# Optimization experiments

Measured on AMD Instinct MI355X. Metric: run time of the kernel, lower is better.

## Reference

```python
import jax, jax.numpy as jnp
import numpy as np

VOCAB, EMB, HID, OUT = 1000, 256, 512, 1
NUM_IN, NUM_OUT = 7, 4
B, S = 64, 512
D = EMB + NUM_OUT  # conv input dim = 260


def setup_inputs() -> dict:
    key = jax.random.key(0)
    ks = jax.random.split(key, 8)
    ev = jax.random.randint(ks[0], (B, S, 1), 0, VOCAB).astype(jnp.float32)
    num = jax.random.normal(ks[1], (B, S, NUM_IN), jnp.float32)
    X = jnp.concatenate([ev, num], axis=-1)  # [B,S,8]; col 0 = event ids
    def w(k, shape, fan_in):
        return jax.random.normal(k, shape, jnp.float32) / np.sqrt(fan_in).astype(np.float32)
    return {
        "X": X,
        "emb": w(ks[2], (VOCAB, EMB), EMB),
        "Wn": w(ks[3], (NUM_IN, NUM_OUT), NUM_IN), "bn": jnp.zeros((NUM_OUT,), jnp.float32),
        "Wf": w(ks[4], (D, 3 * HID), D), "bf": jnp.zeros((3 * HID,), jnp.float32),
        "Wb": w(ks[5], (D, 3 * HID), D), "bb": jnp.zeros((3 * HID,), jnp.float32),
        "Wo": w(ks[6], (2 * HID, OUT), 2 * HID), "bo": jnp.zeros((OUT,), jnp.float32),
    }


def _fo_pool(Z, F):
    # Z, F: [S, B, H]. Linear recurrence h_t = F_t * h_{t-1} + (1 - F_t) * Z_t.
    def step(h, zf):
        z, f = zf
        h = f * h + (1.0 - f) * z
        return h, h
    h0 = jnp.zeros(Z.shape[1:], Z.dtype)
    _, hs = jax.lax.scan(step, h0, (Z, F))
    return hs  # [S, B, H]


def _forward(X, emb, Wn, bn, Wf, bf, Wb, bb, Wo, bo):
    ev = jax.lax.stop_gradient(X[:, :, 0]).astype(jnp.int32)  # event-type ids
    num = X[:, :, 1:]
    e = emb[ev]                          # [B,S,EMB]
    n = num @ Wn + bn                    # [B,S,NUM_OUT]
    c = jnp.concatenate([e, n], axis=-1)  # [B,S,D]

    def gates(W, b):
        g = jnp.einsum('bsd,dk->sbk', c, W) + b  # kernel-1 conv == GEMM; [S,B,3H]
        Z, F = g[..., :HID], g[..., HID:2 * HID]  # O gate is computed but unused upstream
        return jnp.tanh(Z), jax.nn.sigmoid(F)

    Zf, Ff = gates(Wf, bf)
    Zb, Fb = gates(Wb, bb)
    hf = _fo_pool(Zf, Ff)                       # forward direction
    hb = _fo_pool(Zb[::-1], Fb[::-1])[::-1]     # backward: scan reversed, re-reverse
    # torch takes h_combined[-1]: last forward state, first backward-scan state
    final = jnp.concatenate([hf[-1], hb[-1]], axis=-1)  # [B, 2H]
    return final @ Wo + bo  # dropout p=0 is identity


def reference(X, emb, Wn, bn, Wf, bf, Wb, bb, Wo, bo):
    return _forward(X, emb, Wn, bn, Wf, bf, Wb, bb, Wo, bo)
```

## Files before the change

### kernel.cpp

```cpp
#include <hip/hip_runtime.h>
#include <stdint.h>

#define B_ 64
#define S_ 512
#define EMB_ 256
#define NIN_ 7
#define NOUT_ 4
#define HID_ 512
#define VOCAB_ 1000
#define VP_ 1024
#define NG_ 2048
#define M_ (B_ * S_)

typedef __bf16 bf16x8 __attribute__((ext_vector_type(8)));
typedef float floatx4 __attribute__((ext_vector_type(4)));
typedef unsigned short u16x8 __attribute__((ext_vector_type(8)));

__device__ __forceinline__ unsigned short f2bf(float f) {
    unsigned u = __float_as_uint(f);
    u += 0x7FFFu + ((u >> 16) & 1u);
    return (unsigned short)(u >> 16);
}
__device__ __forceinline__ float bf2f(unsigned short h) {
    return __uint_as_float(((unsigned)h) << 16);
}
__device__ __forceinline__ float rcp_(float x) { return __builtin_amdgcn_rcpf(x); }
__device__ __forceinline__ float exp2_(float x) {
    float r; asm("v_exp_f32 %0, %1" : "=v"(r) : "v"(x)); return r;
}
#define L2E_ 1.4426950408889634f
__device__ __forceinline__ float sigmoidf_(float x) {
    return rcp_(1.0f + exp2_(x * (-L2E_)));
}
__device__ __forceinline__ float tanhf_(float x) {
    float ax = fabsf(x);
    float e = exp2_(ax * (-2.0f * L2E_));
    float t = (1.0f - e) * rcp_(1.0f + e);
    return copysignf(t, x);
}


__global__ __launch_bounds__(256) void prep(
    const float* __restrict__ emb, const float* __restrict__ bn,
    const float* __restrict__ Wf, const float* __restrict__ bfv,
    const float* __restrict__ Wb, const float* __restrict__ bb,
    unsigned short* __restrict__ Aemb, unsigned short* __restrict__ WT,
    float* __restrict__ W4, float* __restrict__ bvec) {
    int bid = blockIdx.x;
    int tid = threadIdx.x;

    if (bid < 64) {
        int g = bid;
#pragma unroll
        for (int half = 0; half < 2; ++half) {
            int t = tid + 256 * half;
            int r15 = t & 15;
            int kchunk = (t >> 4) & 3;
            int kt = t >> 6;
            int row = g * 16 + r15;
            int k0 = kt * 32 + kchunk * 8;
            unsigned short p[8];
            if (row < VOCAB_) {
                float4 a = *(const float4*)(emb + (size_t)row * EMB_ + k0);
                float4 b = *(const float4*)(emb + (size_t)row * EMB_ + k0 + 4);
                p[0]=f2bf(a.x); p[1]=f2bf(a.y); p[2]=f2bf(a.z); p[3]=f2bf(a.w);
                p[4]=f2bf(b.x); p[5]=f2bf(b.y); p[6]=f2bf(b.z); p[7]=f2bf(b.w);
            } else {
#pragma unroll
                for (int q = 0; q < 8; ++q) p[q] = 0;
            }
            size_t chunk = ((size_t)(g >> 3) * 8 + kt) * 8 + (g & 7);
            *(u16x8*)(Aemb + chunk * 512 + (16 * kchunk + r15) * 8) =
                *(const u16x8*)p;
        }
    } else if (bid < 80) {
        __shared__ float raw[32][132];
        int idx = bid - 64;
        int p = idx >> 3;
        int gq = idx & 7;
        const float* W = p ? Wb : Wf;
        int j0 = gq * 64;
        int r = tid >> 3;
        int i = tid & 7;

#pragma unroll
        for (int kt = 0; kt < 8; ++kt) {
            int k0 = kt * 32;
            const float* src = W + (size_t)(k0 + r) * 1536;
            float4 a0 = *(const float4*)(src + j0 + i * 8);
            float4 a1 = *(const float4*)(src + j0 + i * 8 + 4);
            float4 b0 = *(const float4*)(src + 512 + j0 + i * 8);
            float4 b1 = *(const float4*)(src + 512 + j0 + i * 8 + 4);
            *(float4*)&raw[r][i * 8]      = a0;
            *(float4*)&raw[r][i * 8 + 4]  = a1;
            *(float4*)&raw[r][64 + i * 8]     = b0;
            *(float4*)&raw[r][64 + i * 8 + 4] = b1;
            __syncthreads();
#pragma unroll
            for (int h = 0; h < 2; ++h) {
                int e = tid + 256 * h;
                int gl = e >> 6;
                int rest = e & 63;
                int kchunk = rest >> 4;
                int v15 = rest & 15;
                int joff = gl * 8 + (v15 >> 1);
                int cl = joff + 64 * (v15 & 1);
                unsigned short pk[8];
#pragma unroll
                for (int q = 0; q < 8; ++q) pk[q] = f2bf(raw[kchunk * 8 + q][cl]);
                int g = p * 64 + gq * 8 + gl;
                size_t chunk = ((size_t)(g >> 3) * 8 + kt) * 8 + (g & 7);
                *(u16x8*)(WT + chunk * 512 + (16 * kchunk + v15) * 8) =
                    *(const u16x8*)pk;
            }
            __syncthreads();
        }
    } else {
        int v = (bid - 80) * 256 + tid;
        int part = v >> 10;
        int m = v & 1023;
        int j = m >> 1;
        int c = (m & 1) ? (512 + j) : j;
        const float* W = part ? Wb : Wf;
        float bv = part ? bb[c] : bfv[c];
#pragma unroll
        for (int q = 0; q < NOUT_; ++q) {
            float w = W[(size_t)(256 + q) * 1536 + c];
            W4[(size_t)q * NG_ + v] = w;
            bv = fmaf(bn[q], w, bv);
        }
        bvec[v] = bv;
    }
}

__global__ __launch_bounds__(256) void gemmG(
    const unsigned short* __restrict__ Aemb, const unsigned short* __restrict__ WT,
    const float* __restrict__ bvec, unsigned short* __restrict__ G) {
    int bid = blockIdx.x;
    int mtile = bid & 7;
    int ntile = bid >> 3;
    int r0 = mtile * 128;
    int n0 = ntile * 128;
    int tid = threadIdx.x;
    int lane = tid & 63, wave = tid >> 6;
    int wm = wave & 1, wn = wave >> 1;
    int rl = lane & 15;

    const unsigned short* pa = Aemb + ((size_t)mtile * 64 + 4 * wm) * 512 + lane * 8;
    const unsigned short* pb = WT + ((size_t)ntile * 64 + 4 * wn) * 512 + lane * 8;

    floatx4 acc[4][4];
#pragma unroll
    for (int mi = 0; mi < 4; ++mi)
#pragma unroll
        for (int ni = 0; ni < 4; ++ni) acc[mi][ni] = (floatx4){0.f, 0.f, 0.f, 0.f};

    bf16x8 afc[4], bfc[4], afn[4], bfn[4];
#pragma unroll
    for (int mi = 0; mi < 4; ++mi) afc[mi] = *(const bf16x8*)(pa + mi * 512);
#pragma unroll
    for (int ni = 0; ni < 4; ++ni) bfc[ni] = *(const bf16x8*)(pb + ni * 512);

#pragma unroll
    for (int kt = 0; kt < 8; ++kt) {
        if (kt < 7) {
#pragma unroll
            for (int mi = 0; mi < 4; ++mi)
                afn[mi] = *(const bf16x8*)(pa + (size_t)(kt + 1) * 4096 + mi * 512);
#pragma unroll
            for (int ni = 0; ni < 4; ++ni)
                bfn[ni] = *(const bf16x8*)(pb + (size_t)(kt + 1) * 4096 + ni * 512);
        }
#pragma unroll
        for (int mi = 0; mi < 4; ++mi)
#pragma unroll
            for (int ni = 0; ni < 4; ++ni)
                acc[mi][ni] = __builtin_amdgcn_mfma_f32_16x16x32_bf16(afc[mi], bfc[ni], acc[mi][ni], 0, 0, 0);
        if (kt < 7) {
#pragma unroll
            for (int mi = 0; mi < 4; ++mi) afc[mi] = afn[mi];
#pragma unroll
            for (int ni = 0; ni < 4; ++ni) bfc[ni] = bfn[ni];
        }
    }

#pragma unroll
    for (int ni = 0; ni < 4; ++ni) {
        int n = n0 + 64 * wn + 16 * ni + rl;
        float bv = bvec[n];
#pragma unroll
        for (int mi = 0; mi < 4; ++mi) {
            int rb = r0 + 64 * wm + 16 * mi + (lane >> 4) * 4;
#pragma unroll
            for (int v = 0; v < 4; ++v)
                G[(size_t)(rb + v) * NG_ + n] = f2bf(acc[mi][ni][v] + bv);
        }
    }
}

__global__ __launch_bounds__(512) void scan(
    const float* __restrict__ X, const unsigned short* __restrict__ G,
    const float* __restrict__ W4, const float* __restrict__ Wn,
    float* __restrict__ PQ) {
    __shared__ float LX[512];
    __shared__ float LN[64][4];
    int bid = blockIdx.x;
    int b = bid >> 3, chunk = bid & 7;
    int s0 = chunk * 64;
    int j = threadIdx.x;

    LX[j] = X[((size_t)b * S_ + s0 + (j >> 3)) * 8 + (j & 7)];
    __syncthreads();

    if (j < 256) {
        int t = j >> 2, q = j & 3;
        float s = 0.f;
#pragma unroll
        for (int i = 0; i < NIN_; ++i) s = fmaf(LX[t * 8 + 1 + i], Wn[i * NOUT_ + q], s);
        LN[t][q] = s;
    }

    float2 w4p[NOUT_];
#pragma unroll
    for (int q = 0; q < NOUT_; ++q)
        w4p[q] = *(const float2*)(W4 + (size_t)q * NG_ + 2 * j);
    __syncthreads();

    float P = 1.f, Q = 0.f;
    int ev0 = (int)LX[0];
    unsigned gpA = *(const unsigned*)(G + (size_t)ev0 * NG_ + 2 * j);
    int ev1 = (int)LX[8];
    unsigned gpB = *(const unsigned*)(G + (size_t)ev1 * NG_ + 2 * j);
#pragma unroll 4
    for (int s = 0; s < 64; ++s) {
        unsigned gpc = gpA;
        gpA = gpB;
        if (s < 62) {
            int evn = (int)LX[(s + 2) * 8];
            gpB = *(const unsigned*)(G + (size_t)evn * NG_ + 2 * j);
        }
        float gz = bf2f((unsigned short)(gpc & 0xffffu));
        float gf = bf2f((unsigned short)(gpc >> 16));
        float4 n4 = *(const float4*)(&LN[s][0]);
        gz = fmaf(n4.x, w4p[0].x, gz);
        gz = fmaf(n4.y, w4p[1].x, gz);
        gz = fmaf(n4.z, w4p[2].x, gz);
        gz = fmaf(n4.w, w4p[3].x, gz);
        gf = fmaf(n4.x, w4p[0].y, gf);
        gf = fmaf(n4.y, w4p[1].y, gf);
        gf = fmaf(n4.z, w4p[2].y, gf);
        gf = fmaf(n4.w, w4p[3].y, gf);
        float z = tanhf_(gz);
        float f = sigmoidf_(gf);
        Q = fmaf(f, Q - z, z);
        P *= f;
    }
    ((float2*)PQ)[(size_t)bid * 512 + j] = make_float2(P, Q);
}

__global__ __launch_bounds__(512) void final_out(
    const float* __restrict__ X, const unsigned short* __restrict__ G,
    const float* __restrict__ W4, const float* __restrict__ Wn,
    const float* __restrict__ Wo, const float* __restrict__ bo,
    const float* __restrict__ PQ, float* __restrict__ out) {
    int b = blockIdx.x;
    int j = threadIdx.x;

    float h = 0.f;
#pragma unroll
    for (int c = 0; c < 8; ++c) {
        float2 pq = ((const float2*)PQ)[((size_t)b * 8 + c) * 512 + j];
        h = fmaf(pq.x, h, pq.y);
    }

    const float* xr = X + ((size_t)b * S_ + (S_ - 1)) * 8;
    int ev = (int)xr[0];
    float n4[NOUT_];
#pragma unroll
    for (int q = 0; q < NOUT_; ++q) {
        float s = 0.f;
#pragma unroll
        for (int i = 0; i < NIN_; ++i) s = fmaf(xr[1 + i], Wn[i * NOUT_ + q], s);
        n4[q] = s;
    }
    unsigned gpc = *(const unsigned*)(G + (size_t)ev * NG_ + 1024 + 2 * j);
    float gz = bf2f((unsigned short)(gpc & 0xffffu));
    float gf = bf2f((unsigned short)(gpc >> 16));
#pragma unroll
    for (int q = 0; q < NOUT_; ++q) {
        float2 w = *(const float2*)(W4 + (size_t)q * NG_ + 1024 + 2 * j);
        gz = fmaf(n4[q], w.x, gz);
        gf = fmaf(n4[q], w.y, gf);
    }
    float hb = (1.f - sigmoidf_(gf)) * tanhf_(gz);

    float partial = fmaf(h, Wo[j], hb * Wo[512 + j]);
#pragma unroll
    for (int off = 32; off > 0; off >>= 1)
        partial += __shfl_down(partial, off);
    __shared__ float red[8];
    if ((j & 63) == 0) red[j >> 6] = partial;
    __syncthreads();
    if (j == 0) {
        float s = bo[0];
#pragma unroll
        for (int w = 0; w < 8; ++w) s += red[w];
        out[b] = s;
    }
}

extern "C" void kernel_launch(void* const* d_in, const int* in_sizes, int n_in,
                              void* d_out, int out_size, void* d_ws, size_t ws_size,
                              hipStream_t stream) {
    const float* X   = (const float*)d_in[0];
    const float* emb = (const float*)d_in[1];
    const float* Wn  = (const float*)d_in[2];
    const float* bn  = (const float*)d_in[3];
    const float* Wf  = (const float*)d_in[4];
    const float* bfv = (const float*)d_in[5];
    const float* Wb  = (const float*)d_in[6];
    const float* bb  = (const float*)d_in[7];
    const float* Wo  = (const float*)d_in[8];
    const float* bo  = (const float*)d_in[9];
    float* out = (float*)d_out;

    size_t off_A  = 0;
    size_t off_WT = off_A  + (size_t)VP_ * EMB_ * 2;
    size_t off_G  = off_WT + (size_t)NG_ * EMB_ * 2;
    size_t off_W4 = off_G  + (size_t)VP_ * NG_ * 2;
    size_t off_bv = off_W4 + (size_t)NOUT_ * NG_ * 4;
    size_t off_PQ = off_bv + (size_t)NG_ * 4;
    size_t need   = off_PQ + (size_t)B_ * 8 * 512 * 2 * sizeof(float);
    if (ws_size < need) return;

    unsigned short* Aemb = (unsigned short*)((char*)d_ws + off_A);
    unsigned short* WT   = (unsigned short*)((char*)d_ws + off_WT);
    unsigned short* G    = (unsigned short*)((char*)d_ws + off_G);
    float*          W4   = (float*)((char*)d_ws + off_W4);
    float*          bvec = (float*)((char*)d_ws + off_bv);
    float*          PQ   = (float*)((char*)d_ws + off_PQ);

    prep<<<88, 256, 0, stream>>>(emb, bn, Wf, bfv, Wb, bb, Aemb, WT, W4, bvec);
    gemmG<<<128, 256, 0, stream>>>(Aemb, WT, bvec, G);
    scan<<<512, 512, 0, stream>>>(X, G, W4, Wn, PQ);
    final_out<<<64, 512, 0, stream>>>(X, G, W4, Wn, Wo, bo, PQ, out);
}
```

Baseline: 109.9 us.

## Fuse four kernels into one persistent megakernel with atomic grid barriers

Merges the prep, GEMM, scan and final kernels into one 512-thread kernel that steps through its phases using global atomic counters as grid-wide barriers. The goal is to remove three kernel launch gaps. The GEMM tile work is split across 8 waves instead of 4, and shared memory is overlaid through a union. It relies on all 512 blocks being co-resident (checked via an occupancy query requiring at least 2 blocks per CU); otherwise it falls back to four phase launches. Spin-waiting and the extra memset add overhead, and if residency does not hold the barriers could deadlock.

After: 110.6 us. Within noise of the previous version (+0.7%).

```diff
diff --git a/kernel.cpp b/kernel.cpp
--- a/kernel.cpp
+++ b/kernel.cpp
@@ -10,7 +10,6 @@
 #define VOCAB_ 1000
 #define VP_ 1024
 #define NG_ 2048
-#define M_ (B_ * S_)
 
 typedef __bf16 bf16x8 __attribute__((ext_vector_type(8)));
 typedef float floatx4 __attribute__((ext_vector_type(4)));
@@ -40,20 +39,44 @@
 }
 
 
-__global__ __launch_bounds__(256) void prep(
-    const float* __restrict__ emb, const float* __restrict__ bn,
+__device__ __forceinline__ void arrive_(unsigned* c) {
+    __syncthreads();
+    if (threadIdx.x == 0)
+        __hip_atomic_fetch_add(c, 1u, __ATOMIC_RELEASE, __HIP_MEMORY_SCOPE_AGENT);
+}
+__device__ __forceinline__ void await_(unsigned* c, unsigned target) {
+    if (threadIdx.x == 0) {
+        while (__hip_atomic_load(c, __ATOMIC_ACQUIRE, __HIP_MEMORY_SCOPE_AGENT) < target)
+            __builtin_amdgcn_s_sleep(16);
+    }
+    __syncthreads();
+}
+
+union ShU {
+    float raw[32][132];
+    struct { float LX[512]; float LN[64][4]; } s;
+    float red[8];
+};
+
+__global__ __launch_bounds__(512, 4) void mega(
+    const float* __restrict__ X, const float* __restrict__ emb,
+    const float* __restrict__ Wn, const float* __restrict__ bn,
     const float* __restrict__ Wf, const float* __restrict__ bfv,
     const float* __restrict__ Wb, const float* __restrict__ bb,
+    const float* __restrict__ Wo, const float* __restrict__ bo,
     unsigned short* __restrict__ Aemb, unsigned short* __restrict__ WT,
-    float* __restrict__ W4, float* __restrict__ bvec) {
-    int bid = blockIdx.x;
-    int tid = threadIdx.x;
-
-    if (bid < 64) {
-        int g = bid;
-#pragma unroll
-        for (int half = 0; half < 2; ++half) {
-            int t = tid + 256 * half;
+    unsigned short* __restrict__ G, float* __restrict__ W4,
+    float* __restrict__ bvec, float* __restrict__ PQ,
+    unsigned* __restrict__ bar, float* __restrict__ out, int phase) {
+    __shared__ ShU U;
+    const int bid = blockIdx.x;
+    const int tid = threadIdx.x;
+    const bool multi = (phase == 0);
+
+    if (multi || phase == 1) {
+        if (bid < 64) {
+            int g = bid;
+            int t = tid;
             int r15 = t & 15;
             int kchunk = (t >> 4) & 3;
             int kt = t >> 6;
@@ -72,240 +95,233 @@
             size_t chunk = ((size_t)(g >> 3) * 8 + kt) * 8 + (g & 7);
             *(u16x8*)(Aemb + chunk * 512 + (16 * kchunk + r15) * 8) =
                 *(const u16x8*)p;
-        }
-    } else if (bid < 80) {
-        __shared__ float raw[32][132];
-        int idx = bid - 64;
-        int p = idx >> 3;
-        int gq = idx & 7;
-        const float* W = p ? Wb : Wf;
-        int j0 = gq * 64;
-        int r = tid >> 3;
-        int i = tid & 7;
+        } else if (bid < 80) {
+            int idx = bid - 64;
+            int p = idx >> 3;
+            int gq = idx & 7;
+            const float* W = p ? Wb : Wf;
+            int j0 = gq * 64;
+            int r = tid >> 3;
+            int i = tid & 7;
+
+#pragma unroll
+            for (int kt = 0; kt < 8; ++kt) {
+                int k0 = kt * 32;
+                if (tid < 256) {
+                    const float* src = W + (size_t)(k0 + r) * 1536;
+                    float4 a0 = *(const float4*)(src + j0 + i * 8);
+                    float4 a1 = *(const float4*)(src + j0 + i * 8 + 4);
+                    float4 b0 = *(const float4*)(src + 512 + j0 + i * 8);
+                    float4 b1 = *(const float4*)(src + 512 + j0 + i * 8 + 4);
+                    *(float4*)&U.raw[r][i * 8]          = a0;
+                    *(float4*)&U.raw[r][i * 8 + 4]      = a1;
+                    *(float4*)&U.raw[r][64 + i * 8]     = b0;
+                    *(float4*)&U.raw[r][64 + i * 8 + 4] = b1;
+                }
+                __syncthreads();
+                {
+                    int e = tid;
+                    int gl = e >> 6;
+                    int rest = e & 63;
+                    int kchunk = rest >> 4;
+                    int v15 = rest & 15;
+                    int joff = gl * 8 + (v15 >> 1);
+                    int cl = joff + 64 * (v15 & 1);
+                    unsigned short pk[8];
+#pragma unroll
+                    for (int q = 0; q < 8; ++q) pk[q] = f2bf(U.raw[kchunk * 8 + q][cl]);
+                    int g = p * 64 + gq * 8 + gl;
+                    size_t chunk = ((size_t)(g >> 3) * 8 + kt) * 8 + (g & 7);
+                    *(u16x8*)(WT + chunk * 512 + (16 * kchunk + v15) * 8) =
+                        *(const u16x8*)pk;
+                }
+                __syncthreads();
+            }
+        } else if (bid < 84) {
+            int v = (bid - 80) * 512 + tid;
+            int part = v >> 10;
+            int m = v & 1023;
+            int j = m >> 1;
+            int c = (m & 1) ? (512 + j) : j;
+            const float* W = part ? Wb : Wf;
+            float bv = part ? bb[c] : bfv[c];
+#pragma unroll
+            for (int q = 0; q < NOUT_; ++q) {
+                float w = W[(size_t)(256 + q) * 1536 + c];
+                W4[(size_t)q * NG_ + v] = w;
+                bv = fmaf(bn[q], w, bv);
+            }
+            bvec[v] = bv;
+        }
+    }
+    if (multi && bid < 84) arrive_(bar + 0);
+
+    if ((multi || phase == 2) && bid < 128) {
+        if (multi) await_(bar + 0, 84u);
+        int mtile = bid & 7;
+        int ntile = bid >> 3;
+        int r0 = mtile * 128;
+        int n0 = ntile * 128;
+        int lane = tid & 63, wave = tid >> 6;
+        int wm = wave & 1;
+        int wn = wave >> 1;
+        int rl = lane & 15;
+
+        const unsigned short* pa = Aemb + ((size_t)mtile * 64 + 4 * wm) * 512 + lane * 8;
+        const unsigned short* pb = WT + ((size_t)ntile * 64 + 2 * wn) * 512 + lane * 8;
+
+        floatx4 acc[4][2];
+#pragma unroll
+        for (int mi = 0; mi < 4; ++mi)
+#pragma unroll
+            for (int ni = 0; ni < 2; ++ni) acc[mi][ni] = (floatx4){0.f, 0.f, 0.f, 0.f};
+
+        bf16x8 afc[4], bfc[2], afn[4], bfn[2];
+#pragma unroll
+        for (int mi = 0; mi < 4; ++mi) afc[mi] = *(const bf16x8*)(pa + mi * 512);
+#pragma unroll
+        for (int ni = 0; ni < 2; ++ni) bfc[ni] = *(const bf16x8*)(pb + ni * 512);
 
 #pragma unroll
         for (int kt = 0; kt < 8; ++kt) {
-            int k0 = kt * 32;
-            const float* src = W + (size_t)(k0 + r) * 1536;
-            float4 a0 = *(const float4*)(src + j0 + i * 8);
-            float4 a1 = *(const float4*)(src + j0 + i * 8 + 4);
-            float4 b0 = *(const float4*)(src + 512 + j0 + i * 8);
-            float4 b1 = *(const float4*)(src + 512 + j0 + i * 8 + 4);
-            *(float4*)&raw[r][i * 8]      = a0;
-            *(float4*)&raw[r][i * 8 + 4]  = a1;
-            *(float4*)&raw[r][64 + i * 8]     = b0;
-            *(float4*)&raw[r][64 + i * 8 + 4] = b1;
-            __syncthreads();
-#pragma unroll
-            for (int h = 0; h < 2; ++h) {
-                int e = tid + 256 * h;
-                int gl = e >> 6;
-                int rest = e & 63;
-                int kchunk = rest >> 4;
-                int v15 = rest & 15;
-                int joff = gl * 8 + (v15 >> 1);
-                int cl = joff + 64 * (v15 & 1);
-                unsigned short pk[8];
-#pragma unroll
-                for (int q = 0; q < 8; ++q) pk[q] = f2bf(raw[kchunk * 8 + q][cl]);
-                int g = p * 64 + gq * 8 + gl;
-                size_t chunk = ((size_t)(g >> 3) * 8 + kt) * 8 + (g & 7);
-                *(u16x8*)(WT + chunk * 512 + (16 * kchunk + v15) * 8) =
-                    *(const u16x8*)pk;
-            }
-            __syncthreads();
-        }
-    } else {
-        int v = (bid - 80) * 256 + tid;
-        int part = v >> 10;
-        int m = v & 1023;
-        int j = m >> 1;
-        int c = (m & 1) ? (512 + j) : j;
-        const float* W = part ? Wb : Wf;
-        float bv = part ? bb[c] : bfv[c];
+            if (kt < 7) {
+#pragma unroll
+                for (int mi = 0; mi < 4; ++mi)
+                    afn[mi] = *(const bf16x8*)(pa + (size_t)(kt + 1) * 4096 + mi * 512);
+#pragma unroll
+                for (int ni = 0; ni < 2; ++ni)
+                    bfn[ni] = *(const bf16x8*)(pb + (size_t)(kt + 1) * 4096 + ni * 512);
+            }
+#pragma unroll
+            for (int mi = 0; mi < 4; ++mi)
+#pragma unroll
+                for (int ni = 0; ni < 2; ++ni)
+                    acc[mi][ni] = __builtin_amdgcn_mfma_f32_16x16x32_bf16(afc[mi], bfc[ni], acc[mi][ni], 0, 0, 0);
+            if (kt < 7) {
+#pragma unroll
+                for (int mi = 0; mi < 4; ++mi) afc[mi] = afn[mi];
+#pragma unroll
+                for (int ni = 0; ni < 2; ++ni) bfc[ni] = bfn[ni];
+            }
+        }
+
+#pragma unroll
+        for (int ni = 0; ni < 2; ++ni) {
+            int n = n0 + 32 * wn + 16 * ni + rl;
+            float bv = bvec[n];
+#pragma unroll
+            for (int mi = 0; mi < 4; ++mi) {
+                int rb = r0 + 64 * wm + 16 * mi + (lane >> 4) * 4;
+#pragma unroll
+                for (int v = 0; v < 4; ++v)
+                    G[(size_t)(rb + v) * NG_ + n] = f2bf(acc[mi][ni][v] + bv);
+            }
+        }
+    }
+    if (multi && bid < 128) arrive_(bar + 1);
+
+    if (multi || phase == 3) {
+        if (multi) await_(bar + 1, 128u);
+        int b = bid >> 3, chunk = bid & 7;
+        int s0 = chunk * 64;
+        int j = tid;
+
+        U.s.LX[j] = X[((size_t)b * S_ + s0 + (j >> 3)) * 8 + (j & 7)];
+        __syncthreads();
+
+        if (j < 256) {
+            int t = j >> 2, q = j & 3;
+            float s = 0.f;
+#pragma unroll
+            for (int i = 0; i < NIN_; ++i)
+                s = fmaf(U.s.LX[t * 8 + 1 + i], Wn[i * NOUT_ + q], s);
+            U.s.LN[t][q] = s;
+        }
+
+        float2 w4p[NOUT_];
+#pragma unroll
+        for (int q = 0; q < NOUT_; ++q)
+            w4p[q] = *(const float2*)(W4 + (size_t)q * NG_ + 2 * j);
+        __syncthreads();
+
+        float P = 1.f, Q = 0.f;
+        int ev0 = (int)U.s.LX[0];
+        unsigned gpA = *(const unsigned*)(G + (size_t)ev0 * NG_ + 2 * j);
+        int ev1 = (int)U.s.LX[8];
+        unsigned gpB = *(const unsigned*)(G + (size_t)ev1 * NG_ + 2 * j);
+#pragma unroll 4
+        for (int s = 0; s < 64; ++s) {
+            unsigned gpc = gpA;
+            gpA = gpB;
+            if (s < 62) {
+                int evn = (int)U.s.LX[(s + 2) * 8];
+                gpB = *(const unsigned*)(G + (size_t)evn * NG_ + 2 * j);
+            }
+            float gz = bf2f((unsigned short)(gpc & 0xffffu));
+            float gf = bf2f((unsigned short)(gpc >> 16));
+            float4 n4 = *(const float4*)(&U.s.LN[s][0]);
+            gz = fmaf(n4.x, w4p[0].x, gz);
+            gz = fmaf(n4.y, w4p[1].x, gz);
+            gz = fmaf(n4.z, w4p[2].x, gz);
+            gz = fmaf(n4.w, w4p[3].x, gz);
+            gf = fmaf(n4.x, w4p[0].y, gf);
+            gf = fmaf(n4.y, w4p[1].y, gf);
+            gf = fmaf(n4.z, w4p[2].y, gf);
+            gf = fmaf(n4.w, w4p[3].y, gf);
+            float z = tanhf_(gz);
+            float f = sigmoidf_(gf);
+            Q = fmaf(f, Q - z, z);
+            P *= f;
+        }
+        ((float2*)PQ)[(size_t)bid * 512 + j] = make_float2(P, Q);
+    }
+    if (multi) arrive_(bar + 2);
+
+    if ((multi || phase == 4) && bid < 64) {
+        if (multi) await_(bar + 2, 512u);
+        int b = bid;
+        int j = tid;
+
+        float h = 0.f;
+#pragma unroll
+        for (int c = 0; c < 8; ++c) {
+            float2 pq = ((const float2*)PQ)[((size_t)b * 8 + c) * 512 + j];
+            h = fmaf(pq.x, h, pq.y);
+        }
+
+        const float* xr = X + ((size_t)b * S_ + (S_ - 1)) * 8;
+        int ev = (int)xr[0];
+        float n4[NOUT_];
 #pragma unroll
         for (int q = 0; q < NOUT_; ++q) {
-            float w = W[(size_t)(256 + q) * 1536 + c];
-            W4[(size_t)q * NG_ + v] = w;
-            bv = fmaf(bn[q], w, bv);
-        }
-        bvec[v] = bv;
-    }
-}
-
-__global__ __launch_bounds__(256) void gemmG(
-    const unsigned short* __restrict__ Aemb, const unsigned short* __restrict__ WT,
-    const float* __restrict__ bvec, unsigned short* __restrict__ G) {
-    int bid = blockIdx.x;
-    int mtile = bid & 7;
-    int ntile = bid >> 3;
-    int r0 = mtile * 128;
-    int n0 = ntile * 128;
-    int tid = threadIdx.x;
-    int lane = tid & 63, wave = tid >> 6;
-    int wm = wave & 1, wn = wave >> 1;
-    int rl = lane & 15;
-
-    const unsigned short* pa = Aemb + ((size_t)mtile * 64 + 4 * wm) * 512 + lane * 8;
-    const unsigned short* pb = WT + ((size_t)ntile * 64 + 4 * wn) * 512 + lane * 8;
-
-    floatx4 acc[4][4];
-#pragma unroll
-    for (int mi = 0; mi < 4; ++mi)
-#pragma unroll
-        for (int ni = 0; ni < 4; ++ni) acc[mi][ni] = (floatx4){0.f, 0.f, 0.f, 0.f};
-
-    bf16x8 afc[4], bfc[4], afn[4], bfn[4];
-#pragma unroll
-    for (int mi = 0; mi < 4; ++mi) afc[mi] = *(const bf16x8*)(pa + mi * 512);
-#pragma unroll
-    for (int ni = 0; ni < 4; ++ni) bfc[ni] = *(const bf16x8*)(pb + ni * 512);
-
-#pragma unroll
-    for (int kt = 0; kt < 8; ++kt) {
-        if (kt < 7) {
-#pragma unroll
-            for (int mi = 0; mi < 4; ++mi)
-                afn[mi] = *(const bf16x8*)(pa + (size_t)(kt + 1) * 4096 + mi * 512);
-#pragma unroll
-            for (int ni = 0; ni < 4; ++ni)
-                bfn[ni] = *(const bf16x8*)(pb + (size_t)(kt + 1) * 4096 + ni * 512);
-        }
-#pragma unroll
-        for (int mi = 0; mi < 4; ++mi)
-#pragma unroll
-            for (int ni = 0; ni < 4; ++ni)
-                acc[mi][ni] = __builtin_amdgcn_mfma_f32_16x16x32_bf16(afc[mi], bfc[ni], acc[mi][ni], 0, 0, 0);
-        if (kt < 7) {
-#pragma unroll
-            for (int mi = 0; mi < 4; ++mi) afc[mi] = afn[mi];
-#pragma unroll
-            for (int ni = 0; ni < 4; ++ni) bfc[ni] = bfn[ni];
-        }
-    }
-
-#pragma unroll
-    for (int ni = 0; ni < 4; ++ni) {
-        int n = n0 + 64 * wn + 16 * ni + rl;
-        float bv = bvec[n];
-#pragma unroll
-        for (int mi = 0; mi < 4; ++mi) {
-            int rb = r0 + 64 * wm + 16 * mi + (lane >> 4) * 4;
-#pragma unroll
-            for (int v = 0; v < 4; ++v)
-                G[(size_t)(rb + v) * NG_ + n] = f2bf(acc[mi][ni][v] + bv);
-        }
-    }
-}
-
-__global__ __launch_bounds__(512) void scan(
-    const float* __restrict__ X, const unsigned short* __restrict__ G,
-    const float* __restrict__ W4, const float* __restrict__ Wn,
-    float* __restrict__ PQ) {
-    __shared__ float LX[512];
-    __shared__ float LN[64][4];
-    int bid = blockIdx.x;
-    int b = bid >> 3, chunk = bid & 7;
-    int s0 = chunk * 64;
-    int j = threadIdx.x;
-
-    LX[j] = X[((size_t)b * S_ + s0 + (j >> 3)) * 8 + (j & 7)];
-    __syncthreads();
-
-    if (j < 256) {
-        int t = j >> 2, q = j & 3;
-        float s = 0.f;
-#pragma unroll
-        for (int i = 0; i < NIN_; ++i) s = fmaf(LX[t * 8 + 1 + i], Wn[i * NOUT_ + q], s);
-        LN[t][q] = s;
-    }
-
-    float2 w4p[NOUT_];
-#pragma unroll
-    for (int q = 0; q < NOUT_; ++q)
-        w4p[q] = *(const float2*)(W4 + (size_t)q * NG_ + 2 * j);
-    __syncthreads();
-
-    float P = 1.f, Q = 0.f;
-    int ev0 = (int)LX[0];
-    unsigned gpA = *(const unsigned*)(G + (size_t)ev0 * NG_ + 2 * j);
-    int ev1 = (int)LX[8];
-    unsigned gpB = *(const unsigned*)(G + (size_t)ev1 * NG_ + 2 * j);
-#pragma unroll 4
-    for (int s = 0; s < 64; ++s) {
-        unsigned gpc = gpA;
-        gpA = gpB;
-        if (s < 62) {
-            int evn = (int)LX[(s + 2) * 8];
-            gpB = *(const unsigned*)(G + (size_t)evn * NG_ + 2 * j);
-        }
+            float s = 0.f;
+#pragma unroll
+            for (int i = 0; i < NIN_; ++i) s = fmaf(xr[1 + i], Wn[i * NOUT_ + q], s);
+            n4[q] = s;
+        }
+        unsigned gpc = *(const unsigned*)(G + (size_t)ev * NG_ + 1024 + 2 * j);
         float gz = bf2f((unsigned short)(gpc & 0xffffu));
         float gf = bf2f((unsigned short)(gpc >> 16));
-        float4 n4 = *(const float4*)(&LN[s][0]);
-        gz = fmaf(n4.x, w4p[0].x, gz);
-        gz = fmaf(n4.y, w4p[1].x, gz);
-        gz = fmaf(n4.z, w4p[2].x, gz);
-        gz = fmaf(n4.w, w4p[3].x, gz);
-        gf = fmaf(n4.x, w4p[0].y, gf);
-        gf = fmaf(n4.y, w4p[1].y, gf);
-        gf = fmaf(n4.z, w4p[2].y, gf);
-        gf = fmaf(n4.w, w4p[3].y, gf);
-        float z = tanhf_(gz);
-        float f = sigmoidf_(gf);
-        Q = fmaf(f, Q - z, z);
-        P *= f;
-    }
-    ((float2*)PQ)[(size_t)bid * 512 + j] = make_float2(P, Q);
-}
-
-__global__ __launch_bounds__(512) void final_out(
-    const float* __restrict__ X, const unsigned short* __restrict__ G,
-    const float* __restrict__ W4, const float* __restrict__ Wn,
-    const float* __restrict__ Wo, const float* __restrict__ bo,
-    const float* __restrict__ PQ, float* __restrict__ out) {
-    int b = blockIdx.x;
-    int j = threadIdx.x;
-
-    float h = 0.f;
-#pragma unroll
-    for (int c = 0; c < 8; ++c) {
-        float2 pq = ((const float2*)PQ)[((size_t)b * 8 + c) * 512 + j];
-        h = fmaf(pq.x, h, pq.y);
-    }
-
-    const float* xr = X + ((size_t)b * S_ + (S_ - 1)) * 8;
-    int ev = (int)xr[0];
-    float n4[NOUT_];
-#pragma unroll
-    for (int q = 0; q < NOUT_; ++q) {
-        float s = 0.f;
-#pragma unroll
-        for (int i = 0; i < NIN_; ++i) s = fmaf(xr[1 + i], Wn[i * NOUT_ + q], s);
-        n4[q] = s;
-    }
-    unsigned gpc = *(const unsigned*)(G + (size_t)ev * NG_ + 1024 + 2 * j);
-    float gz = bf2f((unsigned short)(gpc & 0xffffu));
-    float gf = bf2f((unsigned short)(gpc >> 16));
-#pragma unroll
-    for (int q = 0; q < NOUT_; ++q) {
-        float2 w = *(const float2*)(W4 + (size_t)q * NG_ + 1024 + 2 * j);
-        gz = fmaf(n4[q], w.x, gz);
-        gf = fmaf(n4[q], w.y, gf);
-    }
-    float hb = (1.f - sigmoidf_(gf)) * tanhf_(gz);
-
-    float partial = fmaf(h, Wo[j], hb * Wo[512 + j]);
-#pragma unroll
-    for (int off = 32; off > 0; off >>= 1)
-        partial += __shfl_down(partial, off);
-    __shared__ float red[8];
-    if ((j & 63) == 0) red[j >> 6] = partial;
-    __syncthreads();
-    if (j == 0) {
-        float s = bo[0];
-#pragma unroll
-        for (int w = 0; w < 8; ++w) s += red[w];
-        out[b] = s;
+#pragma unroll
+        for (int q = 0; q < NOUT_; ++q) {
+            float2 w = *(const float2*)(W4 + (size_t)q * NG_ + 1024 + 2 * j);
+            gz = fmaf(n4[q], w.x, gz);
+            gf = fmaf(n4[q], w.y, gf);
+        }
+        float hb = (1.f - sigmoidf_(gf)) * tanhf_(gz);
+
+        float partial = fmaf(h, Wo[j], hb * Wo[512 + j]);
+#pragma unroll
+        for (int off = 32; off > 0; off >>= 1)
+            partial += __shfl_down(partial, off);
+        if ((j & 63) == 0) U.red[j >> 6] = partial;
+        __syncthreads();
+        if (j == 0) {
+            float s = bo[0];
+#pragma unroll
+            for (int w = 0; w < 8; ++w) s += U.red[w];
+            out[b] = s;
+        }
     }
 }
 
@@ -324,13 +340,14 @@
     const float* bo  = (const float*)d_in[9];
     float* out = (float*)d_out;
 
-    size_t off_A  = 0;
-    size_t off_WT = off_A  + (size_t)VP_ * EMB_ * 2;
-    size_t off_G  = off_WT + (size_t)NG_ * EMB_ * 2;
-    size_t off_W4 = off_G  + (size_t)VP_ * NG_ * 2;
-    size_t off_bv = off_W4 + (size_t)NOUT_ * NG_ * 4;
-    size_t off_PQ = off_bv + (size_t)NG_ * 4;
-    size_t need   = off_PQ + (size_t)B_ * 8 * 512 * 2 * sizeof(float);
+    size_t off_A   = 0;
+    size_t off_WT  = off_A  + (size_t)VP_ * EMB_ * 2;
+    size_t off_G   = off_WT + (size_t)NG_ * EMB_ * 2;
+    size_t off_W4  = off_G  + (size_t)VP_ * NG_ * 2;
+    size_t off_bv  = off_W4 + (size_t)NOUT_ * NG_ * 4;
+    size_t off_PQ  = off_bv + (size_t)NG_ * 4;
+    size_t off_bar = off_PQ + (size_t)B_ * 8 * 512 * 2 * sizeof(float);
+    size_t need    = off_bar + 16;
     if (ws_size < need) return;
 
     unsigned short* Aemb = (unsigned short*)((char*)d_ws + off_A);
@@ -339,9 +356,22 @@
     float*          W4   = (float*)((char*)d_ws + off_W4);
     float*          bvec = (float*)((char*)d_ws + off_bv);
     float*          PQ   = (float*)((char*)d_ws + off_PQ);
-
-    prep<<<88, 256, 0, stream>>>(emb, bn, Wf, bfv, Wb, bb, Aemb, WT, W4, bvec);
-    gemmG<<<128, 256, 0, stream>>>(Aemb, WT, bvec, G);
-    scan<<<512, 512, 0, stream>>>(X, G, W4, Wn, PQ);
-    final_out<<<64, 512, 0, stream>>>(X, G, W4, Wn, Wo, bo, PQ, out);
-}
+    unsigned*       bar  = (unsigned*)((char*)d_ws + off_bar);
+
+    static int coop = -1;
+    if (coop < 0) {
+        int nb = 0;
+        hipError_t e = hipOccupancyMaxActiveBlocksPerMultiprocessor(&nb, mega, 512, 0);
+        coop = (e == hipSuccess && nb >= 2) ? 1 : 0;
+    }
+
+    hipMemsetAsync((char*)d_ws + off_bar, 0, 16, stream);
+    if (coop) {
+        mega<<<512, 512, 0, stream>>>(X, emb, Wn, bn, Wf, bfv, Wb, bb, Wo, bo,
+                                      Aemb, WT, G, W4, bvec, PQ, bar, out, 0);
+    } else {
+        for (int p = 1; p <= 4; ++p)
+            mega<<<512, 512, 0, stream>>>(X, emb, Wn, bn, Wf, bfv, Wb, bb, Wo, bo,
+                                          Aemb, WT, G, W4, bvec, PQ, bar, out, p);
+    }
+}
```
